# Kernel optimization log

Hardware: AMD Instinct MI355X
Metric: run time of the kernel (lower is better)

The kernel has to match this reference:

```python
import jax, jax.numpy as jnp
import numpy as np

WINDOW_SIZE = 2
MAX_POW = 3


def setup_inputs() -> dict:
    return {"t": 8, "h": 32, "w": 32}


def reference(t, h, w):
    N = t * h * w
    grid = jnp.stack(
        jnp.meshgrid(jnp.arange(t), jnp.arange(h), jnp.arange(w), indexing="ij"),
        axis=-1,
    ).reshape(N, 3)
    # [N, N, 3] absolute coordinate differences
    abs_diff = jnp.abs(grid[:, None, :] - grid[None, :, :])

    # Local window: all three axis-diffs within window_size
    mask_local = jnp.all(abs_diff <= WINDOW_SIZE, axis=-1)

    # Dilated sparse: along exactly one axis, diff in {2^0,...,2^(max_pow-1)},
    # other two axes equal. Single pass instead of max_pow*3 OR'd NxN temporaries.
    offsets = 2 ** jnp.arange(MAX_POW)  # [1, 2, 4]
    is_pow = jnp.any(abs_diff[..., :, None] == offsets, axis=-1)  # [N, N, 3]
    is_zero = abs_diff == 0  # [N, N, 3]
    mask_sparse = (
        (is_pow[..., 0] & is_zero[..., 1] & is_zero[..., 2])
        | (is_pow[..., 1] & is_zero[..., 0] & is_zero[..., 2])
        | (is_pow[..., 2] & is_zero[..., 0] & is_zero[..., 1])
    )

    mask_combined = mask_local | mask_sparse
    neg_inf = jnp.finfo(jnp.float32).min
    return jnp.where(mask_combined, jnp.float32(0.0), neg_inf)
```

## Files before the change

kernel.cpp:

```cpp
#include <hip/hip_runtime.h>
#include <cmath>

#define NEG_MASKED (-3.3895313892515355e+38f)

typedef float v4f __attribute__((ext_vector_type(4)));

__global__ __launch_bounds__(256) void mask_rows(
    const int* __restrict__ hp, const int* __restrict__ wp,
    float* __restrict__ out, int N) {
  const int h = hp[0];
  const int w = wp[0];
  const int hw = h * w;

  const int i = blockIdx.x;
  float* __restrict__ row = out + (size_t)i * (size_t)N;

  if ((N & 3) == 0) {
    const v4f c = {NEG_MASKED, NEG_MASKED, NEG_MASKED, NEG_MASKED};
    v4f* __restrict__ r4 = (v4f*)row;
    const int n4 = N >> 2;
    for (int k = threadIdx.x; k < n4; k += 256)
      r4[k] = c;
  } else {
    for (int k = threadIdx.x; k < N; k += 256)
      row[k] = NEG_MASKED;
  }

  __syncthreads();

  const int k = threadIdx.x;
  if (k >= 131) return;

  const int ti = i / hw;
  const int ir = i - ti * hw;
  const int hi = ir / w;
  const int wi = ir - hi * w;

  int dt, dh, dw;
  if (k < 125) {
    dw = k % 5 - 2;
    dh = (k / 5) % 5 - 2;
    dt = k / 25 - 2;
  } else {
    const int e = k - 125;
    const int s = (e & 1) ? 4 : -4;
    dt = dh = dw = 0;
    if (e < 2)      dt = s;
    else if (e < 4) dh = s;
    else            dw = s;
  }

  const int hj = hi + dh;
  const int wj = wi + dw;
  const int j = i + dt * hw + dh * w + dw;
  if (((unsigned)hj < (unsigned)h) & ((unsigned)wj < (unsigned)w) &
      ((unsigned)j < (unsigned)N))
    row[j] = 0.0f;
}

extern "C" void kernel_launch(void* const* d_in, const int* in_sizes, int n_in,
                              void* d_out, int out_size, void* d_ws, size_t ws_size,
                              hipStream_t stream) {
  const int* hp = (const int*)d_in[1];
  const int* wp = (const int*)d_in[2];
  float* out = (float*)d_out;

  const long long os = (long long)out_size;
  int N = (int)floor(sqrt((double)os));
  while ((long long)(N + 1) * (long long)(N + 1) <= os) ++N;
  while ((long long)N * (long long)N > os) --N;
  if (N < 1) N = 1;

  mask_rows<<<dim3(N), dim3(256), 0, stream>>>(hp, wp, out, N);
}
```

Measured before the change: 257.3 us.

## Split mask into grid-stride nontemporal fill plus vectorized per-row fixup kernel

Replaces the single per-row kernel with two launches: a grid-stride fill kernel that writes the masked value with nontemporal vector stores, and a fixup kernel that overwrites only the allowed entries. In the common case the fixup writes aligned 16-byte vectors covering each window segment instead of scattered scalar stores. This targets the write bandwidth of the 256 MB output and the per-row barrier. In exchange it adds a second launch, rewrites some cache lines, and depends on the fill finishing before the fixup through stream ordering.

Result: slower. 302.3 us (+17.5%).

```diff
diff --git a/kernel.cpp b/kernel.cpp
--- a/kernel.cpp
+++ b/kernel.cpp
@@ -5,7 +5,20 @@
 
 typedef float v4f __attribute__((ext_vector_type(4)));
 
-__global__ __launch_bounds__(256) void mask_rows(
+__global__ __launch_bounds__(256) void fill_neg(float* __restrict__ out,
+                                                long long n4, long long total) {
+  const v4f c = {NEG_MASKED, NEG_MASKED, NEG_MASKED, NEG_MASKED};
+  v4f* __restrict__ o4 = (v4f*)out;
+  const long long idx = (long long)blockIdx.x * 256ll + (long long)threadIdx.x;
+  const long long stride = (long long)gridDim.x * 256ll;
+  for (long long k = idx; k < n4; k += stride)
+    __builtin_nontemporal_store(c, o4 + k);
+  if (idx == 0)
+    for (long long k = n4 * 4ll; k < total; ++k)
+      out[k] = NEG_MASKED;
+}
+
+__global__ __launch_bounds__(256) void fixup_rows(
     const int* __restrict__ hp, const int* __restrict__ wp,
     float* __restrict__ out, int N) {
   const int h = hp[0];
@@ -13,49 +26,85 @@
   const int hw = h * w;
 
   const int i = blockIdx.x;
+  const int tid = threadIdx.x;
   float* __restrict__ row = out + (size_t)i * (size_t)N;
-
-  if ((N & 3) == 0) {
-    const v4f c = {NEG_MASKED, NEG_MASKED, NEG_MASKED, NEG_MASKED};
-    v4f* __restrict__ r4 = (v4f*)row;
-    const int n4 = N >> 2;
-    for (int k = threadIdx.x; k < n4; k += 256)
-      r4[k] = c;
-  } else {
-    for (int k = threadIdx.x; k < N; k += 256)
-      row[k] = NEG_MASKED;
-  }
-
-  __syncthreads();
-
-  const int k = threadIdx.x;
-  if (k >= 131) return;
 
   const int ti = i / hw;
   const int ir = i - ti * hw;
   const int hi = ir / w;
   const int wi = ir - hi * w;
 
-  int dt, dh, dw;
-  if (k < 125) {
-    dw = k % 5 - 2;
-    dh = (k / 5) % 5 - 2;
-    dt = k / 25 - 2;
+  const bool fast = ((N & 15) == 0) & (h >= 5) &
+                    ((((w & 15) == 0) & (w >= 32)) | (w >= 48)) &
+                    (hw >= 4 * w + 64);
+
+  if (fast) {
+    int s, p;
+    if (tid < 200)      { s = tid >> 3; p = tid & 7; }
+    else if (tid < 216) { s = 25 + ((tid - 200) >> 2); p = (tid - 200) & 3; }
+    else return;
+
+    int c, base;
+    bool isCenter = false, validSeg = true, isSingle = false;
+    if (s < 25) {
+      const int dt = s / 5 - 2, dh = s % 5 - 2;
+      isCenter = (s == 12);
+      c = i + dt * hw + dh * w;
+      validSeg = ((unsigned)(hi + dh) < (unsigned)h);
+      base = (c - 4) & ~15;
+    } else if (s < 27) {
+      c = i + ((s == 25) ? -4 : 4) * hw;
+      base = c & ~15;
+      isSingle = true;
+    } else {
+      const int dh = (s == 27) ? -4 : 4;
+      c = i + dh * w;
+      validSeg = ((unsigned)(hi + dh) < (unsigned)h);
+      base = c & ~15;
+      isSingle = true;
+    }
+    if (!validSeg) return;
+    const int col0 = base + p * 4;
+    if ((unsigned)col0 >= (unsigned)N) return;
+
+    v4f v;
+#pragma unroll
+    for (int e = 0; e < 4; ++e) {
+      const int d = col0 + e - c;
+      bool kept;
+      if (isSingle) {
+        kept = (d == 0);
+      } else {
+        const int ad = abs(d);
+        kept = ((ad <= 2) | (isCenter & (ad == 4))) &
+               ((unsigned)(wi + d) < (unsigned)w);
+      }
+      v[e] = kept ? 0.0f : NEG_MASKED;
+    }
+    *(v4f*)(row + col0) = v;
   } else {
-    const int e = k - 125;
-    const int s = (e & 1) ? 4 : -4;
-    dt = dh = dw = 0;
-    if (e < 2)      dt = s;
-    else if (e < 4) dh = s;
-    else            dw = s;
+    const int k = tid;
+    if (k >= 131) return;
+    int dt, dh, dw;
+    if (k < 125) {
+      dw = k % 5 - 2;
+      dh = (k / 5) % 5 - 2;
+      dt = k / 25 - 2;
+    } else {
+      const int e = k - 125;
+      const int sgn = (e & 1) ? 4 : -4;
+      dt = dh = dw = 0;
+      if (e < 2)      dt = sgn;
+      else if (e < 4) dh = sgn;
+      else            dw = sgn;
+    }
+    const int hj = hi + dh;
+    const int wj = wi + dw;
+    const int j = i + dt * hw + dh * w + dw;
+    if (((unsigned)hj < (unsigned)h) & ((unsigned)wj < (unsigned)w) &
+        ((unsigned)j < (unsigned)N))
+      row[j] = 0.0f;
   }
-
-  const int hj = hi + dh;
-  const int wj = wi + dw;
-  const int j = i + dt * hw + dh * w + dw;
-  if (((unsigned)hj < (unsigned)h) & ((unsigned)wj < (unsigned)w) &
-      ((unsigned)j < (unsigned)N))
-    row[j] = 0.0f;
 }
 
 extern "C" void kernel_launch(void* const* d_in, const int* in_sizes, int n_in,
@@ -71,5 +120,13 @@
   while ((long long)N * (long long)N > os) --N;
   if (N < 1) N = 1;
 
-  mask_rows<<<dim3(N), dim3(256), 0, stream>>>(hp, wp, out, N);
+  const long long total = (long long)N * (long long)N;
+  const long long n4 = total / 4;
+
+  long long want = (n4 + 255) / 256;
+  if (want < 1) want = 1;
+  const int blocks = (want > 2048ll) ? 2048 : (int)want;
+  fill_neg<<<dim3(blocks), dim3(256), 0, stream>>>(out, n4, total);
+
+  fixup_rows<<<dim3(N), dim3(256), 0, stream>>>(hp, wp, out, N);
 }
```
